# Performance work log

Hardware: AMD Instinct MI355X
Metric: run time of the kernel (lower is better)

Reference implementation:

```python
import jax, jax.numpy as jnp
import numpy as np

B, T, C = 512, 256, 384
HEAD = 64

def setup_inputs() -> dict:
    key = jax.random.key(0)
    k1, k2, k3, k4 = jax.random.split(key, 4)
    x = jax.random.normal(k1, (B, T, C), dtype=jnp.float32)
    Wq = jax.random.normal(k2, (C, HEAD), dtype=jnp.float32) * (C ** -0.5)
    Wk = jax.random.normal(k3, (C, HEAD), dtype=jnp.float32) * (C ** -0.5)
    Wv = jax.random.normal(k4, (C, HEAD), dtype=jnp.float32) * (C ** -0.5)
    return {"x": x, "Wq": Wq, "Wk": Wk, "Wv": Wv}

def reference(x, Wq, Wk, Wv):
    # projections (Linear with bias=False): x @ W
    q = jnp.einsum('btc,ch->bth', x, Wq)   # [B,T,H]
    k = jnp.einsum('btc,ch->bth', x, Wk)   # [B,T,H]
    v = jnp.einsum('btc,ch->bth', x, Wv)   # [B,T,H]
    Cdim = x.shape[-1]
    # NOTE: original scales by C**-0.5 where C = nEmbd (not headSize)
    scores = jnp.einsum('bth,bsh->bts', q, k) * (Cdim ** -0.5)  # [B,T,T]
    Tlen = x.shape[1]
    causal = jnp.tril(jnp.ones((Tlen, Tlen), dtype=bool))
    scores = jnp.where(causal, scores, -jnp.inf)
    wei = jax.nn.softmax(scores, axis=-1)
    # dropout omitted (eval mode / deterministic reference)
    out = jnp.einsum('bts,bsh->bth', wei, v)  # [B,T,H]
    return out
```

## Files before the change

kernel.cpp:

```cpp
#include <hip/hip_runtime.h>

#define B_ 512
#define T_ 256
#define C_ 384
#define H_ 64

typedef __bf16 bf16;
typedef bf16  bf16x8 __attribute__((ext_vector_type(8)));
typedef float f32x4  __attribute__((ext_vector_type(4)));

#define NCHUNK     3
#define CHUNK_K    128
#define WT3_CHUNK  24576
#define WT3_TOTAL  (NCHUNK * WT3_CHUNK)

__global__ void prep_wt3(const float* __restrict__ Wq,
                         const float* __restrict__ Wk,
                         const float* __restrict__ Wv,
                         bf16* __restrict__ wt3)
{
    int idx = blockIdx.x * 256 + threadIdx.x;
    if (idx >= WT3_TOTAL) return;
    int chunk = idx / WT3_CHUNK;
    int rem   = idx % WT3_CHUNK;
    int s     = rem >> 3;
    int e     = rem & 7;
    int mc    = s >> 4;
    int kkc   = (s & 15) ^ (mc & 7);
    int mat   = mc >> 6;
    int col   = mc & 63;
    int k     = chunk * CHUNK_K + kkc * 8 + e;
    const float* W = (mat == 0) ? Wq : (mat == 1) ? Wk : Wv;
    wt3[idx] = (bf16)W[k * H_ + col];
}

__device__ __forceinline__ bf16x8 cvt8(float4 a, float4 b)
{
    bf16x8 r;
    r[0] = (bf16)a.x; r[1] = (bf16)a.y; r[2] = (bf16)a.z; r[3] = (bf16)a.w;
    r[4] = (bf16)b.x; r[5] = (bf16)b.y; r[6] = (bf16)b.z; r[7] = (bf16)b.w;
    return r;
}

__device__ __forceinline__ void gload_lds16(const bf16* g, bf16* l)
{
    __builtin_amdgcn_global_load_lds(
        (const __attribute__((address_space(1))) void*)g,
        (__attribute__((address_space(3))) void*)l,
        16, 0, 0);
}

#define SWZ(row, col) ((col) ^ (((row) & 7) << 3))

__device__ __forceinline__ const bf16x8* wts_frag(const bf16* wt_s, int mc, int kk)
{
    int byte = ((mc * CHUNK_K + kk) * 2) ^ ((mc & 7) << 4);
    return reinterpret_cast<const bf16x8*>(reinterpret_cast<const char*>(wt_s) + byte);
}

template<int USE_WT>
__global__ __launch_bounds__(512, 2)
void head_fused11(const float* __restrict__ x,
                  const float* __restrict__ Wq,
                  const float* __restrict__ Wk,
                  const float* __restrict__ Wv,
                  const bf16* __restrict__ wt3,
                  float* __restrict__ out)
{
    __shared__ bf16 lds_u[32768];
    __shared__ bf16 p_s[8 * 16 * 64];

    bf16* wt_s = lds_u;
    bf16* k_s  = lds_u;
    bf16* vT_s = lds_u + 16384;

    const int tid  = threadIdx.x;
    const int wave = tid >> 6;
    const int lane = tid & 63;
    const int lr   = lane & 15;
    const int lg   = lane >> 4;

    const int b = blockIdx.x;
    const float* xb = x + (size_t)b * T_ * C_;
    bf16* pw = &p_s[wave * 16 * 64];

    const int mt0 = wave, mt1 = 15 - wave;
    bf16x8 qf[2][2];

    f32x4 acc[2][3][4];
    #pragma unroll
    for (int t = 0; t < 2; ++t)
        #pragma unroll
        for (int a = 0; a < 3; ++a)
            #pragma unroll
            for (int nw = 0; nw < 4; ++nw)
                acc[t][a][nw] = (f32x4){0.f, 0.f, 0.f, 0.f};

    #pragma unroll 1
    for (int chunk = 0; chunk < NCHUNK; ++chunk) {
        if (chunk) __syncthreads();
        if (USE_WT) {
            #pragma unroll
            for (int c = 0; c < 6; ++c) {
                const bf16* g = wt3 + chunk * WT3_CHUNK + (c * 512 + tid) * 8;
                bf16* l = wt_s + (c * 512 + wave * 64) * 8;
                gload_lds16(g, l);
            }
        } else {
            #pragma unroll
            for (int c = 0; c < 6; ++c) {
                int f16 = c * 512 + tid;
                int mc  = f16 >> 4;
                int kkc = f16 & 15;
                int mat = mc >> 6, col = mc & 63;
                const float* W = (mat == 0) ? Wq : (mat == 1) ? Wk : Wv;
                bf16x8 vv;
                #pragma unroll
                for (int j = 0; j < 8; ++j)
                    vv[j] = (bf16)W[(chunk * CHUNK_K + kkc * 8 + j) * H_ + col];
                int byte = ((mc * CHUNK_K + kkc * 8) * 2) ^ ((mc & 7) << 4);
                *reinterpret_cast<bf16x8*>(reinterpret_cast<char*>(wt_s) + byte) = vv;
            }
        }
        __syncthreads();

        const float* xr0 = xb + (mt0 * 16 + lr) * C_ + chunk * CHUNK_K + lg * 8;
        const float* xr1 = xb + (mt1 * 16 + lr) * C_ + chunk * CHUNK_K + lg * 8;
        #pragma unroll
        for (int ks = 0; ks < 4; ++ks) {
            float4 a0 = *reinterpret_cast<const float4*>(xr0 + ks * 32);
            float4 a1 = *reinterpret_cast<const float4*>(xr0 + ks * 32 + 4);
            float4 b0 = *reinterpret_cast<const float4*>(xr1 + ks * 32);
            float4 b1 = *reinterpret_cast<const float4*>(xr1 + ks * 32 + 4);
            bf16x8 af0 = cvt8(a0, a1);
            bf16x8 af1 = cvt8(b0, b1);
            const int kk = ks * 32 + lg * 8;
            #pragma unroll
            for (int mat = 0; mat < 3; ++mat) {
                #pragma unroll
                for (int nw = 0; nw < 4; ++nw) {
                    bf16x8 bfr = *wts_frag(wt_s, mat * 64 + nw * 16 + lr, kk);
                    acc[0][mat][nw] = __builtin_amdgcn_mfma_f32_16x16x32_bf16(
                        af0, bfr, acc[0][mat][nw], 0, 0, 0);
                    acc[1][mat][nw] = __builtin_amdgcn_mfma_f32_16x16x32_bf16(
                        af1, bfr, acc[1][mat][nw], 0, 0, 0);
                }
            }
        }
    }
    __syncthreads();

    #pragma unroll
    for (int tile = 0; tile < 2; ++tile) {
        const int mt = tile ? mt1 : mt0;
        #pragma unroll
        for (int nw = 0; nw < 4; ++nw) {
            #pragma unroll
            for (int r = 0; r < 4; ++r) {
                int row = mt * 16 + lg * 4 + r;
                int col = nw * 16 + lr;
                k_s[row * 64 + SWZ(row, col)]   = (bf16)acc[tile][1][nw][r];
                vT_s[col * 256 + SWZ(col, row)] = (bf16)acc[tile][2][nw][r];
            }
        }
        #pragma unroll
        for (int nw = 0; nw < 4; ++nw) {
            #pragma unroll
            for (int r = 0; r < 4; ++r) {
                int row = lg * 4 + r;
                pw[row * 64 + SWZ(row, nw * 16 + lr)] = (bf16)acc[tile][0][nw][r];
            }
        }
        asm volatile("s_waitcnt lgkmcnt(0)" ::: "memory");
        __builtin_amdgcn_sched_barrier(0);
        qf[tile][0] = *reinterpret_cast<const bf16x8*>(&pw[lr * 64 + SWZ(lr, lg * 8)]);
        qf[tile][1] = *reinterpret_cast<const bf16x8*>(&pw[lr * 64 + SWZ(lr, 32 + lg * 8)]);
        asm volatile("s_waitcnt lgkmcnt(0)" ::: "memory");
        __builtin_amdgcn_sched_barrier(0);
    }
    __syncthreads();

    const float scale = 0.051031036307982884f;

    #pragma unroll
    for (int p = 0; p < 2; ++p) {
        const int mt  = p ? mt1 : mt0;
        const int nkt = mt + 1;

        float m[4], l[4];
        f32x4 oacc[4];
        #pragma unroll
        for (int r = 0; r < 4; ++r) { m[r] = -1e30f; l[r] = 0.f; }
        #pragma unroll
        for (int n = 0; n < 4; ++n) oacc[n] = (f32x4){0.f, 0.f, 0.f, 0.f};

        #pragma unroll
        for (int h = 0; h < 2; ++h) {
            const int vh = (nkt - h * 8) < 8 ? (nkt - h * 8) : 8;
            if (vh > 0) {
                float s[8][4];
                #pragma unroll
                for (int j = 0; j < 8; ++j) {
                    const int kt = h * 8 + j;
                    if (j < vh) {
                        bf16x8 kf0 = *reinterpret_cast<const bf16x8*>(
                            &k_s[(kt * 16 + lr) * 64 + SWZ(lr, lg * 8)]);
                        bf16x8 kf1 = *reinterpret_cast<const bf16x8*>(
                            &k_s[(kt * 16 + lr) * 64 + SWZ(lr, 32 + lg * 8)]);
                        f32x4 sc = (f32x4){0.f, 0.f, 0.f, 0.f};
                        sc = __builtin_amdgcn_mfma_f32_16x16x32_bf16(qf[p][0], kf0, sc, 0, 0, 0);
                        sc = __builtin_amdgcn_mfma_f32_16x16x32_bf16(qf[p][1], kf1, sc, 0, 0, 0);
                        #pragma unroll
                        for (int r = 0; r < 4; ++r) {
                            float v = sc[r] * scale;
                            if (kt == mt && lr > lg * 4 + r) v = -1e30f;
                            s[j][r] = v;
                        }
                    } else {
                        #pragma unroll
                        for (int r = 0; r < 4; ++r) s[j][r] = -1e30f;
                    }
                }

                float f[4];
                #pragma unroll
                for (int r = 0; r < 4; ++r) {
                    float pm = s[0][r];
                    #pragma unroll
                    for (int j = 1; j < 8; ++j) pm = fmaxf(pm, s[j][r]);
                    pm = fmaxf(pm, __shfl_xor(pm, 1));
                    pm = fmaxf(pm, __shfl_xor(pm, 2));
                    pm = fmaxf(pm, __shfl_xor(pm, 4));
                    pm = fmaxf(pm, __shfl_xor(pm, 8));
                    float nm = fmaxf(m[r], pm);
                    f[r] = __expf(m[r] - nm);
                    m[r] = nm;
                    l[r] *= f[r];
                }
                #pragma unroll
                for (int n = 0; n < 4; ++n)
                    #pragma unroll
                    for (int r = 0; r < 4; ++r)
                        oacc[n][r] *= f[r];

                #pragma unroll
                for (int r = 0; r < 4; ++r) {
                    float t = 0.f;
                    #pragma unroll
                    for (int j = 0; j < 8; ++j) {
                        float e = __expf(s[j][r] - m[r]);
                        s[j][r] = e;
                        t += e;
                    }
                    t += __shfl_xor(t, 1);
                    t += __shfl_xor(t, 2);
                    t += __shfl_xor(t, 4);
                    t += __shfl_xor(t, 8);
                    l[r] += t;
                }

                const int nkk = (vh + 1) >> 1;
                #pragma unroll
                for (int kkl = 0; kkl < 4; ++kkl) {
                    if (kkl < nkk) {
                        const int kk = h * 4 + kkl;
                        #pragma unroll
                        for (int r = 0; r < 4; ++r) {
                            int row = lg * 4 + r;
                            pw[row * 64 + SWZ(row, lr)]      = (bf16)s[2 * kkl][r];
                            pw[row * 64 + SWZ(row, 16 + lr)] = (bf16)s[2 * kkl + 1][r];
                        }
                        asm volatile("s_waitcnt lgkmcnt(0)" ::: "memory");
                        __builtin_amdgcn_sched_barrier(0);
                        bf16x8 pf = *reinterpret_cast<const bf16x8*>(
                            &pw[lr * 64 + SWZ(lr, lg * 8)]);
                        #pragma unroll
                        for (int n = 0; n < 4; ++n) {
                            bf16x8 vf = *reinterpret_cast<const bf16x8*>(
                                &vT_s[(n * 16 + lr) * 256 + SWZ(lr, kk * 32 + lg * 8)]);
                            oacc[n] = __builtin_amdgcn_mfma_f32_16x16x32_bf16(pf, vf, oacc[n], 0, 0, 0);
                        }
                    }
                }
            }
        }

        float rin[4];
        #pragma unroll
        for (int r = 0; r < 4; ++r) rin[r] = 1.0f / l[r];
        float* op = out + ((size_t)b * T_ + mt * 16) * H_;
        #pragma unroll
        for (int n = 0; n < 4; ++n)
            #pragma unroll
            for (int r = 0; r < 4; ++r)
                op[(lg * 4 + r) * H_ + n * 16 + lr] = oacc[n][r] * rin[r];
    }
}

extern "C" void kernel_launch(void* const* d_in, const int* in_sizes, int n_in,
                              void* d_out, int out_size, void* d_ws, size_t ws_size,
                              hipStream_t stream)
{
    (void)in_sizes; (void)n_in; (void)out_size;
    const float* x  = (const float*)d_in[0];
    const float* Wq = (const float*)d_in[1];
    const float* Wk = (const float*)d_in[2];
    const float* Wv = (const float*)d_in[3];
    float* o = (float*)d_out;

    if (ws_size >= (size_t)(WT3_TOTAL * sizeof(bf16))) {
        bf16* wt3 = (bf16*)d_ws;
        prep_wt3<<<dim3((WT3_TOTAL + 255) / 256), dim3(256), 0, stream>>>(Wq, Wk, Wv, wt3);
        head_fused11<1><<<dim3(B_), dim3(512), 0, stream>>>(x, Wq, Wk, Wv, wt3, o);
    } else {
        head_fused11<0><<<dim3(B_), dim3(512), 0, stream>>>(x, Wq, Wk, Wv, nullptr, o);
    }
}
```

Before: 66.85 us.

## Compute transposed attention scores and shuffle P in registers instead of LDS

Swaps the MFMA operand order so each lane holds one query row's scores across its accumulator entries. Per-row max and sum then need only two cross-lane shuffles, and the output can be written with float4 stores. The P matrix for the PV product is rebuilt in registers with packed bf16 shuffles, removing the LDS write, wait and read round-trip per step. In exchange it adds several ds_bpermute shuffles and selects per step.

```diff
diff --git a/kernel.cpp b/kernel.cpp
--- a/kernel.cpp
+++ b/kernel.cpp
@@ -7,7 +7,9 @@
 
 typedef __bf16 bf16;
 typedef bf16  bf16x8 __attribute__((ext_vector_type(8)));
+typedef bf16  bf16x2 __attribute__((ext_vector_type(2)));
 typedef float f32x4  __attribute__((ext_vector_type(4)));
+typedef int   i32x4  __attribute__((ext_vector_type(4)));
 
 #define NCHUNK     3
 #define CHUNK_K    128
@@ -42,6 +44,12 @@
     return r;
 }
 
+__device__ __forceinline__ unsigned pack2(float a, float b)
+{
+    bf16x2 v; v[0] = (bf16)a; v[1] = (bf16)b;
+    return __builtin_bit_cast(unsigned, v);
+}
+
 __device__ __forceinline__ void gload_lds16(const bf16* g, bf16* l)
 {
     __builtin_amdgcn_global_load_lds(
@@ -60,7 +68,7 @@
 
 template<int USE_WT>
 __global__ __launch_bounds__(512, 2)
-void head_fused11(const float* __restrict__ x,
+void head_fused12(const float* __restrict__ x,
                   const float* __restrict__ Wq,
                   const float* __restrict__ Wk,
                   const float* __restrict__ Wv,
@@ -187,10 +195,8 @@
         const int mt  = p ? mt1 : mt0;
         const int nkt = mt + 1;
 
-        float m[4], l[4];
+        float m = -1e30f, l = 0.f;
         f32x4 oacc[4];
-        #pragma unroll
-        for (int r = 0; r < 4; ++r) { m[r] = -1e30f; l[r] = 0.f; }
         #pragma unroll
         for (int n = 0; n < 4; ++n) oacc[n] = (f32x4){0.f, 0.f, 0.f, 0.f};
 
@@ -208,12 +214,12 @@
                         bf16x8 kf1 = *reinterpret_cast<const bf16x8*>(
                             &k_s[(kt * 16 + lr) * 64 + SWZ(lr, 32 + lg * 8)]);
                         f32x4 sc = (f32x4){0.f, 0.f, 0.f, 0.f};
-                        sc = __builtin_amdgcn_mfma_f32_16x16x32_bf16(qf[p][0], kf0, sc, 0, 0, 0);
-                        sc = __builtin_amdgcn_mfma_f32_16x16x32_bf16(qf[p][1], kf1, sc, 0, 0, 0);
+                        sc = __builtin_amdgcn_mfma_f32_16x16x32_bf16(kf0, qf[p][0], sc, 0, 0, 0);
+                        sc = __builtin_amdgcn_mfma_f32_16x16x32_bf16(kf1, qf[p][1], sc, 0, 0, 0);
                         #pragma unroll
                         for (int r = 0; r < 4; ++r) {
                             float v = sc[r] * scale;
-                            if (kt == mt && lr > lg * 4 + r) v = -1e30f;
+                            if (kt == mt && (lg * 4 + r) > lr) v = -1e30f;
                             s[j][r] = v;
                         }
                     } else {
@@ -222,78 +228,79 @@
                     }
                 }
 
-                float f[4];
-                #pragma unroll
-                for (int r = 0; r < 4; ++r) {
-                    float pm = s[0][r];
+                float pm = s[0][0];
+                #pragma unroll
+                for (int j = 0; j < 8; ++j)
                     #pragma unroll
-                    for (int j = 1; j < 8; ++j) pm = fmaxf(pm, s[j][r]);
-                    pm = fmaxf(pm, __shfl_xor(pm, 1));
-                    pm = fmaxf(pm, __shfl_xor(pm, 2));
-                    pm = fmaxf(pm, __shfl_xor(pm, 4));
-                    pm = fmaxf(pm, __shfl_xor(pm, 8));
-                    float nm = fmaxf(m[r], pm);
-                    f[r] = __expf(m[r] - nm);
-                    m[r] = nm;
-                    l[r] *= f[r];
-                }
+                    for (int r = 0; r < 4; ++r) pm = fmaxf(pm, s[j][r]);
+                pm = fmaxf(pm, __shfl_xor(pm, 16));
+                pm = fmaxf(pm, __shfl_xor(pm, 32));
+                float nm = fmaxf(m, pm);
+                float fr = __expf(m - nm);
+                m = nm;
+                l *= fr;
                 #pragma unroll
                 for (int n = 0; n < 4; ++n)
                     #pragma unroll
-                    for (int r = 0; r < 4; ++r)
-                        oacc[n][r] *= f[r];
-
-                #pragma unroll
-                for (int r = 0; r < 4; ++r) {
-                    float t = 0.f;
+                    for (int r = 0; r < 4; ++r) oacc[n][r] *= fr;
+
+                float tt = 0.f;
+                #pragma unroll
+                for (int j = 0; j < 8; ++j)
                     #pragma unroll
-                    for (int j = 0; j < 8; ++j) {
-                        float e = __expf(s[j][r] - m[r]);
+                    for (int r = 0; r < 4; ++r) {
+                        float e = __expf(s[j][r] - m);
                         s[j][r] = e;
-                        t += e;
+                        tt += e;
                     }
-                    t += __shfl_xor(t, 1);
-                    t += __shfl_xor(t, 2);
-                    t += __shfl_xor(t, 4);
-                    t += __shfl_xor(t, 8);
-                    l[r] += t;
-                }
+                tt += __shfl_xor(tt, 16);
+                tt += __shfl_xor(tt, 32);
+                l += tt;
 
                 const int nkk = (vh + 1) >> 1;
                 #pragma unroll
                 for (int kkl = 0; kkl < 4; ++kkl) {
                     if (kkl < nkk) {
                         const int kk = h * 4 + kkl;
-                        #pragma unroll
-                        for (int r = 0; r < 4; ++r) {
-                            int row = lg * 4 + r;
-                            pw[row * 64 + SWZ(row, lr)]      = (bf16)s[2 * kkl][r];
-                            pw[row * 64 + SWZ(row, 16 + lr)] = (bf16)s[2 * kkl + 1][r];
-                        }
-                        asm volatile("s_waitcnt lgkmcnt(0)" ::: "memory");
-                        __builtin_amdgcn_sched_barrier(0);
-                        bf16x8 pf = *reinterpret_cast<const bf16x8*>(
-                            &pw[lr * 64 + SWZ(lr, lg * 8)]);
+                        unsigned lo0 = pack2(s[2*kkl][0],   s[2*kkl][1]);
+                        unsigned hi0 = pack2(s[2*kkl][2],   s[2*kkl][3]);
+                        unsigned lo1 = pack2(s[2*kkl+1][0], s[2*kkl+1][1]);
+                        unsigned hi1 = pack2(s[2*kkl+1][2], s[2*kkl+1][3]);
+                        const int src0 = (lg & 1) * 32 + lr;
+                        const int src1 = src0 + 16;
+                        const bool t1  = (lg >> 1) != 0;
+                        int a0 = __shfl((int)lo0, src0), a1 = __shfl((int)lo1, src0);
+                        unsigned w0 = t1 ? (unsigned)a1 : (unsigned)a0;
+                        int b0 = __shfl((int)hi0, src0), b1 = __shfl((int)hi1, src0);
+                        unsigned w1 = t1 ? (unsigned)b1 : (unsigned)b0;
+                        int c0 = __shfl((int)lo0, src1), c1 = __shfl((int)lo1, src1);
+                        unsigned w2 = t1 ? (unsigned)c1 : (unsigned)c0;
+                        int d0 = __shfl((int)hi0, src1), d1 = __shfl((int)hi1, src1);
+                        unsigned w3 = t1 ? (unsigned)d1 : (unsigned)d0;
+                        i32x4 wi = {(int)w0, (int)w1, (int)w2, (int)w3};
+                        bf16x8 pf = __builtin_bit_cast(bf16x8, wi);
                         #pragma unroll
                         for (int n = 0; n < 4; ++n) {
                             bf16x8 vf = *reinterpret_cast<const bf16x8*>(
                                 &vT_s[(n * 16 + lr) * 256 + SWZ(lr, kk * 32 + lg * 8)]);
-                            oacc[n] = __builtin_amdgcn_mfma_f32_16x16x32_bf16(pf, vf, oacc[n], 0, 0, 0);
+                            oacc[n] = __builtin_amdgcn_mfma_f32_16x16x32_bf16(vf, pf, oacc[n], 0, 0, 0);
                         }
                     }
                 }
             }
         }
 
-        float rin[4];
-        #pragma unroll
-        for (int r = 0; r < 4; ++r) rin[r] = 1.0f / l[r];
-        float* op = out + ((size_t)b * T_ + mt * 16) * H_;
-        #pragma unroll
-        for (int n = 0; n < 4; ++n)
-            #pragma unroll
-            for (int r = 0; r < 4; ++r)
-                op[(lg * 4 + r) * H_ + n * 16 + lr] = oacc[n][r] * rin[r];
+        const float rin = 1.0f / l;
+        float* op = out + ((size_t)b * T_ + mt * 16 + lr) * H_;
+        #pragma unroll
+        for (int n = 0; n < 4; ++n) {
+            float4 st;
+            st.x = oacc[n][0] * rin;
+            st.y = oacc[n][1] * rin;
+            st.z = oacc[n][2] * rin;
+            st.w = oacc[n][3] * rin;
+            *reinterpret_cast<float4*>(op + n * 16 + lg * 4) = st;
+        }
     }
 }
 
@@ -311,8 +318,8 @@
     if (ws_size >= (size_t)(WT3_TOTAL * sizeof(bf16))) {
         bf16* wt3 = (bf16*)d_ws;
         prep_wt3<<<dim3((WT3_TOTAL + 255) / 256), dim3(256), 0, stream>>>(Wq, Wk, Wv, wt3);
-        head_fused11<1><<<dim3(B_), dim3(512), 0, stream>>>(x, Wq, Wk, Wv, wt3, o);
+        head_fused12<1><<<dim3(B_), dim3(512), 0, stream>>>(x, Wq, Wk, Wv, wt3, o);
     } else {
-        head_fused11<0><<<dim3(B_), dim3(512), 0, stream>>>(x, Wq, Wk, Wv, nullptr, o);
+        head_fused12<0><<<dim3(B_), dim3(512), 0, stream>>>(x, Wq, Wk, Wv, nullptr, o);
     }
 }
```

Result: faster. 64.91 us (-2.9%).
